# Kernel optimization log

Hardware: AMD Instinct MI355X
Metric: run time of the kernel (lower is better)

Reference implementation:

```python
import jax, jax.numpy as jnp
import numpy as np

B, N, D = 256, 2048, 256

def setup_inputs() -> dict:
    key = jax.random.key(0)
    k1, k2, k3, k4 = jax.random.split(key, 4)
    feature = jax.random.normal(k1, (B, N, D), dtype=jnp.float32)
    pointer_hidden_state = jax.random.normal(k2, (B, D), dtype=jnp.float32)
    # learned params (match torch.randn init)
    v = jax.random.normal(k3, (1, 1, D), dtype=jnp.float32)
    W = jax.random.normal(k4, (1, D, 2 * D), dtype=jnp.float32)
    return {"feature": feature, "pointer_hidden_state": pointer_hidden_state, "v": v, "W": W}

def reference(feature, pointer_hidden_state, v, W):
    # hidden: concat(feature, broadcast hidden state) -> [B, N, 2D]
    b, n, d = feature.shape
    h = jnp.broadcast_to(pointer_hidden_state[:, None, :], (b, n, d))
    hidden = jnp.concatenate([feature, h], axis=2)            # [B, N, 2D]
    # W @ hidden^T fused as einsum: [D, 2D] x [B, N, 2D] -> [B, N, D]
    pre = jnp.tanh(jnp.einsum('de,bne->bnd', W[0], hidden))
    # v . pre -> [B, N]
    scores = jnp.einsum('d,bnd->bn', v[0, 0], pre)
    attns = jax.nn.softmax(scores, axis=1)[:, None, :]        # [B, 1, N]
    return attns
```

## Files before the change

### kernel.cpp

```cpp
#include <hip/hip_runtime.h>
#include <hip/hip_fp16.h>

typedef _Float16 f16;
typedef _Float16 f16x4 __attribute__((ext_vector_type(4)));
typedef _Float16 f16x8 __attribute__((ext_vector_type(8)));
typedef float f32x4 __attribute__((ext_vector_type(4)));

#define NCH 64
#define CHB 32768
#define PLB 16384
#define PSTRIDE 524288

#define BAR()     asm volatile("s_waitcnt lgkmcnt(0)\n\ts_barrier" ::: "memory")
#define WAITV_(N) asm volatile("s_waitcnt vmcnt(" #N ")" ::: "memory")
#define WAITV(N)  WAITV_(N)

__global__ void prep_w(const float* __restrict__ W, f16* __restrict__ wbuf) {
    int idx = blockIdx.x * 256 + threadIdx.x;
    int d = idx >> 8, k = idx & 255;
    float w = W[d * 512 + k];
    int ct   = d >> 4;
    int lane = (d & 15) | (((k >> 3) & 3) << 4);
    int ks   = k >> 5;
    int j    = k & 7;
    wbuf[(((ks * 16 + ct) * 64) + lane) * 8 + j] = (f16)w;
}

__global__ void prep_c(const float* __restrict__ W, const float* __restrict__ h,
                       float* __restrict__ c) {
    __shared__ float hs[256];
    int b = blockIdx.x, d = threadIdx.x;
    hs[d] = h[b * 256 + d];
    __syncthreads();
    const float4* w4 = (const float4*)(W + d * 512 + 256);
    const float4* h4 = (const float4*)hs;
    float acc = 0.f;
#pragma unroll 8
    for (int e = 0; e < 64; ++e) {
        float4 a = w4[e], bb = h4[e];
        acc += a.x * bb.x + a.y * bb.y + a.z * bb.z + a.w * bb.w;
    }
    c[b * 256 + d] = acc;
}

__global__ __launch_bounds__(512, 2)
void main_gemm(const float* __restrict__ feat, const f16* __restrict__ wbuf,
               const float* __restrict__ cb, const float* __restrict__ vvec,
               float* __restrict__ psc) {
    __shared__ __align__(16) char rawb[2 * CHB];
    __shared__ __align__(16) char plnb[2 * PLB];

    const int tid = threadIdx.x;
    const int w = tid >> 6;
    const int l = tid & 63;
    const int g = l >> 4;
    const int lr = l & 15;
    const int rh = w >> 2;
    const int cg = w & 3;
    const int b = blockIdx.x;

    f16x8 wf[4][8];
    {
        const f16x8* wp = (const f16x8*)wbuf;
#pragma unroll
        for (int ct = 0; ct < 4; ++ct) {
            int ctg = cg * 4 + ct;
#pragma unroll
            for (int ks = 0; ks < 8; ++ks)
                wf[ct][ks] = wp[(ks * 16 + ctg) * 64 + l];
        }
    }
    float c_[4], v_[4];
#pragma unroll
    for (int ct = 0; ct < 4; ++ct) {
        c_[ct] = cb[b * 256 + (cg * 4 + ct) * 16 + lr];
        v_[ct] = vvec[(cg * 4 + ct) * 16 + lr];
    }

    const char* tbb = (const char*)(feat + (size_t)b * 2048 * 256);

#define ISSUE(u)                                                                   \
    {                                                                              \
        const char* nb = tbb + (size_t)(u) * CHB;                                  \
        char* Q = rawb + ((u) & 1) * CHB;                                          \
        _Pragma("unroll")                                                          \
        for (int i = 0; i < 4; ++i)                                                \
            __builtin_amdgcn_global_load_lds(                                      \
                (const __attribute__((address_space(1))) void*)(nb + i * 8192 + tid * 16), \
                (__attribute__((address_space(3))) void*)(Q + i * 8192 + tid * 16),\
                16, 0, 0);                                                         \
    }

    const int ck0 = (tid & 63) * 4;
    int cvt_off[4];
#pragma unroll
    for (int r = 0; r < 4; ++r) {
        int row = r * 8 + w;
        cvt_off[r] = (((row * 512 + (ck0 & ~7) * 2) ^ ((row & 7) << 4)) +
                      ((ck0 & 4) << 1));
    }

#define CVT(u)                                                                     \
    {                                                                              \
        const char* rp = rawb + ((u) & 1) * CHB;                                   \
        char* hq = plnb + ((u) & 1) * PLB;                                         \
        _Pragma("unroll")                                                          \
        for (int r = 0; r < 4; ++r) {                                              \
            f32x4 x = *(const f32x4*)(rp + r * 8192 + tid * 16);                   \
            f16x4 hv = {(f16)x[0], (f16)x[1], (f16)x[2], (f16)x[3]};               \
            *(f16x4*)(hq + cvt_off[r]) = hv;                                       \
        }                                                                          \
    }

    const int arow = rh * 16 + lr;
    const int aswz = (arow & 7) << 4;

    ISSUE(0); ISSUE(1);
    WAITV(4);
    CVT(0);

    for (int t = 0; t < NCH; ++t) {
        BAR();
        if (t + 2 < NCH) ISSUE(t + 2);

        const char* hp = plnb + (t & 1) * PLB;
        f32x4 acc[4] = {};
#pragma unroll
        for (int ks = 0; ks < 8; ++ks) {
            int ao = (arow * 512 + ks * 64 + g * 16) ^ aswz;
            f16x8 ahi = *(const f16x8*)(hp + ao);
            acc[0] = __builtin_amdgcn_mfma_f32_16x16x32_f16(ahi, wf[0][ks], acc[0], 0, 0, 0);
            acc[1] = __builtin_amdgcn_mfma_f32_16x16x32_f16(ahi, wf[1][ks], acc[1], 0, 0, 0);
            acc[2] = __builtin_amdgcn_mfma_f32_16x16x32_f16(ahi, wf[2][ks], acc[2], 0, 0, 0);
            acc[3] = __builtin_amdgcn_mfma_f32_16x16x32_f16(ahi, wf[3][ks], acc[3], 0, 0, 0);
        }

        float s[4];
#pragma unroll
        for (int r = 0; r < 4; ++r) {
            float a = 0.f;
#pragma unroll
            for (int ct = 0; ct < 4; ++ct) {
                float x = acc[ct][r] + c_[ct];
                float tnh = 1.f - __fdividef(2.f, __expf(2.f * x) + 1.f);
                a += v_[ct] * tnh;
            }
            s[r] = a;
        }
#pragma unroll
        for (int m = 1; m < 16; m <<= 1) {
            s[0] += __shfl_xor(s[0], m, 64);
            s[1] += __shfl_xor(s[1], m, 64);
            s[2] += __shfl_xor(s[2], m, 64);
            s[3] += __shfl_xor(s[3], m, 64);
        }

        if (t < NCH - 2)      WAITV(4);
        else if (t == NCH - 2) WAITV(0);
        if (t + 1 < NCH) CVT(t + 1);

        if (lr == 0) {
            size_t rowg = (size_t)b * 2048 + t * 32 + rh * 16 + g * 4;
            float4 o = {s[0], s[1], s[2], s[3]};
            *(float4*)(psc + (size_t)cg * PSTRIDE + rowg) = o;
        }
    }
#undef ISSUE
#undef CVT
}

__global__ void softmax_k(const float* __restrict__ psc, float* __restrict__ out) {
    __shared__ float red[16];
    int b = blockIdx.x, tid = threadIdx.x;
    float sc[8];
    float m = -3.4e38f;
#pragma unroll
    for (int q = 0; q < 8; ++q) {
        size_t row = (size_t)b * 2048 + q * 256 + tid;
        sc[q] = (psc[row] + psc[PSTRIDE + row]) +
                (psc[2 * PSTRIDE + row] + psc[3 * PSTRIDE + row]);
        m = fmaxf(m, sc[q]);
    }
#pragma unroll
    for (int d = 1; d < 64; d <<= 1) m = fmaxf(m, __shfl_xor(m, d, 64));
    if ((tid & 63) == 0) red[tid >> 6] = m;
    __syncthreads();
    m = fmaxf(fmaxf(red[0], red[1]), fmaxf(red[2], red[3]));
    float e[8], sum = 0.f;
#pragma unroll
    for (int q = 0; q < 8; ++q) { e[q] = __expf(sc[q] - m); sum += e[q]; }
#pragma unroll
    for (int d = 1; d < 64; d <<= 1) sum += __shfl_xor(sum, d, 64);
    if ((tid & 63) == 0) red[8 + (tid >> 6)] = sum;
    __syncthreads();
    sum = (red[8] + red[9]) + (red[10] + red[11]);
    float inv = __fdividef(1.f, sum);
#pragma unroll
    for (int q = 0; q < 8; ++q)
        out[(size_t)b * 2048 + q * 256 + tid] = e[q] * inv;
}

extern "C" void kernel_launch(void* const* d_in, const int* in_sizes, int n_in,
                              void* d_out, int out_size, void* d_ws, size_t ws_size,
                              hipStream_t stream) {
    const float* feat = (const float*)d_in[0];
    const float* h    = (const float*)d_in[1];
    const float* v    = (const float*)d_in[2];
    const float* W    = (const float*)d_in[3];
    float* out = (float*)d_out;

    f16*   wbuf = (f16*)d_ws;
    float* cbuf = (float*)((char*)d_ws + 131072);
    float* psc  = (float*)((char*)d_ws + 524288);

    prep_w<<<256, 256, 0, stream>>>(W, wbuf);
    prep_c<<<256, 256, 0, stream>>>(W, h, cbuf);
    main_gemm<<<256, 512, 0, stream>>>(feat, wbuf, cbuf, v, psc);
    softmax_k<<<256, 256, 0, stream>>>(psc, out);
}
```

Before: 167.7 us.

## Fuse weight prep, bias compute, GEMM and softmax into a single kernel

Collapses four launches into one kernel. Each block now converts its W fragments to fp16 and computes its bias vector c from W and the hidden state, instead of relying on separate prep kernels. Partial scores are reduced across column groups in shared memory, and the softmax over N runs at the end of the same block, removing the global partial-score round trip and the separate softmax launch. In exchange, every block redundantly reads and converts W (256 blocks × 512 KB of mostly L2-resident data), and LDS usage rises by about 10 KB per block, which could affect the two-blocks-per-CU occupancy.

```diff
diff --git a/kernel.cpp b/kernel.cpp
--- a/kernel.cpp
+++ b/kernel.cpp
@@ -9,46 +9,22 @@
 #define NCH 64
 #define CHB 32768
 #define PLB 16384
-#define PSTRIDE 524288
 
 #define BAR()     asm volatile("s_waitcnt lgkmcnt(0)\n\ts_barrier" ::: "memory")
 #define WAITV_(N) asm volatile("s_waitcnt vmcnt(" #N ")" ::: "memory")
 #define WAITV(N)  WAITV_(N)
 
-__global__ void prep_w(const float* __restrict__ W, f16* __restrict__ wbuf) {
-    int idx = blockIdx.x * 256 + threadIdx.x;
-    int d = idx >> 8, k = idx & 255;
-    float w = W[d * 512 + k];
-    int ct   = d >> 4;
-    int lane = (d & 15) | (((k >> 3) & 3) << 4);
-    int ks   = k >> 5;
-    int j    = k & 7;
-    wbuf[(((ks * 16 + ct) * 64) + lane) * 8 + j] = (f16)w;
-}
-
-__global__ void prep_c(const float* __restrict__ W, const float* __restrict__ h,
-                       float* __restrict__ c) {
-    __shared__ float hs[256];
-    int b = blockIdx.x, d = threadIdx.x;
-    hs[d] = h[b * 256 + d];
-    __syncthreads();
-    const float4* w4 = (const float4*)(W + d * 512 + 256);
-    const float4* h4 = (const float4*)hs;
-    float acc = 0.f;
-#pragma unroll 8
-    for (int e = 0; e < 64; ++e) {
-        float4 a = w4[e], bb = h4[e];
-        acc += a.x * bb.x + a.y * bb.y + a.z * bb.z + a.w * bb.w;
-    }
-    c[b * 256 + d] = acc;
-}
-
 __global__ __launch_bounds__(512, 2)
-void main_gemm(const float* __restrict__ feat, const f16* __restrict__ wbuf,
-               const float* __restrict__ cb, const float* __restrict__ vvec,
-               float* __restrict__ psc) {
+void fused(const float* __restrict__ feat, const float* __restrict__ hvec,
+           const float* __restrict__ vvec, const float* __restrict__ W,
+           float* __restrict__ out) {
     __shared__ __align__(16) char rawb[2 * CHB];
     __shared__ __align__(16) char plnb[2 * PLB];
+    __shared__ __align__(16) float pbuf[2][32][4];
+    __shared__ __align__(16) float sbuf[2048];
+    __shared__ __align__(16) float hs[256];
+    __shared__ __align__(16) float cl[256];
+    __shared__ float red[16];
 
     const int tid = threadIdx.x;
     const int w = tid >> 6;
@@ -59,35 +35,56 @@
     const int cg = w & 3;
     const int b = blockIdx.x;
 
+    if (tid < 256) hs[tid] = hvec[b * 256 + tid];
+    __syncthreads();
+
+    {
+        int d = tid >> 1, half = tid & 1;
+        const float4* w4 = (const float4*)(W + d * 512 + 256 + half * 128);
+        const float4* h4 = (const float4*)(hs + half * 128);
+        float a = 0.f;
+#pragma unroll 8
+        for (int e = 0; e < 32; ++e) {
+            float4 x = w4[e], y = h4[e];
+            a += x.x * y.x + x.y * y.y + x.z * y.z + x.w * y.w;
+        }
+        a += __shfl_xor(a, 1, 64);
+        if (half == 0) cl[d] = a;
+    }
+
     f16x8 wf[4][8];
-    {
-        const f16x8* wp = (const f16x8*)wbuf;
-#pragma unroll
-        for (int ct = 0; ct < 4; ++ct) {
-            int ctg = cg * 4 + ct;
-#pragma unroll
-            for (int ks = 0; ks < 8; ++ks)
-                wf[ct][ks] = wp[(ks * 16 + ctg) * 64 + l];
-        }
-    }
-    float c_[4], v_[4];
 #pragma unroll
     for (int ct = 0; ct < 4; ++ct) {
-        c_[ct] = cb[b * 256 + (cg * 4 + ct) * 16 + lr];
-        v_[ct] = vvec[(cg * 4 + ct) * 16 + lr];
-    }
+        int d = (cg * 4 + ct) * 16 + lr;
+        const float* wr = W + d * 512 + g * 8;
+#pragma unroll
+        for (int ks = 0; ks < 8; ++ks) {
+            float4 a0 = *(const float4*)(wr + ks * 32);
+            float4 a1 = *(const float4*)(wr + ks * 32 + 4);
+            f16x8 hv = {(f16)a0.x, (f16)a0.y, (f16)a0.z, (f16)a0.w,
+                        (f16)a1.x, (f16)a1.y, (f16)a1.z, (f16)a1.w};
+            wf[ct][ks] = hv;
+        }
+    }
+    float v_[4];
+#pragma unroll
+    for (int ct = 0; ct < 4; ++ct) v_[ct] = vvec[(cg * 4 + ct) * 16 + lr];
+    __syncthreads();
+    float c_[4];
+#pragma unroll
+    for (int ct = 0; ct < 4; ++ct) c_[ct] = cl[(cg * 4 + ct) * 16 + lr];
 
     const char* tbb = (const char*)(feat + (size_t)b * 2048 * 256);
 
 #define ISSUE(u)                                                                   \
     {                                                                              \
-        const char* nb = tbb + (size_t)(u) * CHB;                                  \
-        char* Q = rawb + ((u) & 1) * CHB;                                          \
+        const char* nb_ = tbb + (size_t)(u) * CHB;                                 \
+        char* Q_ = rawb + ((u) & 1) * CHB;                                         \
         _Pragma("unroll")                                                          \
-        for (int i = 0; i < 4; ++i)                                                \
+        for (int i_ = 0; i_ < 4; ++i_)                                             \
             __builtin_amdgcn_global_load_lds(                                      \
-                (const __attribute__((address_space(1))) void*)(nb + i * 8192 + tid * 16), \
-                (__attribute__((address_space(3))) void*)(Q + i * 8192 + tid * 16),\
+                (const __attribute__((address_space(1))) void*)(nb_ + i_ * 8192 + tid * 16), \
+                (__attribute__((address_space(3))) void*)(Q_ + i_ * 8192 + tid * 16),\
                 16, 0, 0);                                                         \
     }
 
@@ -102,13 +99,13 @@
 
 #define CVT(u)                                                                     \
     {                                                                              \
-        const char* rp = rawb + ((u) & 1) * CHB;                                   \
-        char* hq = plnb + ((u) & 1) * PLB;                                         \
+        const char* rp_ = rawb + ((u) & 1) * CHB;                                  \
+        char* hq_ = plnb + ((u) & 1) * PLB;                                        \
         _Pragma("unroll")                                                          \
         for (int r = 0; r < 4; ++r) {                                              \
-            f32x4 x = *(const f32x4*)(rp + r * 8192 + tid * 16);                   \
-            f16x4 hv = {(f16)x[0], (f16)x[1], (f16)x[2], (f16)x[3]};               \
-            *(f16x4*)(hq + cvt_off[r]) = hv;                                       \
+            f32x4 x_ = *(const f32x4*)(rp_ + r * 8192 + tid * 16);                 \
+            f16x4 hv_ = {(f16)x_[0], (f16)x_[1], (f16)x_[2], (f16)x_[3]};          \
+            *(f16x4*)(hq_ + cvt_off[r]) = hv_;                                     \
         }                                                                          \
     }
 
@@ -122,6 +119,12 @@
     for (int t = 0; t < NCH; ++t) {
         BAR();
         if (t + 2 < NCH) ISSUE(t + 2);
+
+        if (t > 0 && w == ((t - 1) & 7) && l < 32) {
+            const float* pb_ = &pbuf[(t - 1) & 1][l][0];
+            f32x4 p_ = *(const f32x4*)pb_;
+            sbuf[(t - 1) * 32 + l] = (p_[0] + p_[1]) + (p_[2] + p_[3]);
+        }
 
         const char* hp = plnb + (t & 1) * PLB;
         f32x4 acc[4] = {};
@@ -160,44 +163,46 @@
         if (t + 1 < NCH) CVT(t + 1);
 
         if (lr == 0) {
-            size_t rowg = (size_t)b * 2048 + t * 32 + rh * 16 + g * 4;
-            float4 o = {s[0], s[1], s[2], s[3]};
-            *(float4*)(psc + (size_t)cg * PSTRIDE + rowg) = o;
+            int r0 = rh * 16 + g * 4;
+            pbuf[t & 1][r0 + 0][cg] = s[0];
+            pbuf[t & 1][r0 + 1][cg] = s[1];
+            pbuf[t & 1][r0 + 2][cg] = s[2];
+            pbuf[t & 1][r0 + 3][cg] = s[3];
         }
     }
 #undef ISSUE
 #undef CVT
-}
-
-__global__ void softmax_k(const float* __restrict__ psc, float* __restrict__ out) {
-    __shared__ float red[16];
-    int b = blockIdx.x, tid = threadIdx.x;
-    float sc[8];
-    float m = -3.4e38f;
-#pragma unroll
-    for (int q = 0; q < 8; ++q) {
-        size_t row = (size_t)b * 2048 + q * 256 + tid;
-        sc[q] = (psc[row] + psc[PSTRIDE + row]) +
-                (psc[2 * PSTRIDE + row] + psc[3 * PSTRIDE + row]);
-        m = fmaxf(m, sc[q]);
-    }
-#pragma unroll
-    for (int d = 1; d < 64; d <<= 1) m = fmaxf(m, __shfl_xor(m, d, 64));
-    if ((tid & 63) == 0) red[tid >> 6] = m;
-    __syncthreads();
-    m = fmaxf(fmaxf(red[0], red[1]), fmaxf(red[2], red[3]));
-    float e[8], sum = 0.f;
-#pragma unroll
-    for (int q = 0; q < 8; ++q) { e[q] = __expf(sc[q] - m); sum += e[q]; }
-#pragma unroll
-    for (int d = 1; d < 64; d <<= 1) sum += __shfl_xor(sum, d, 64);
-    if ((tid & 63) == 0) red[8 + (tid >> 6)] = sum;
-    __syncthreads();
-    sum = (red[8] + red[9]) + (red[10] + red[11]);
-    float inv = __fdividef(1.f, sum);
-#pragma unroll
-    for (int q = 0; q < 8; ++q)
-        out[(size_t)b * 2048 + q * 256 + tid] = e[q] * inv;
+
+    BAR();
+    if (w == ((NCH - 1) & 7) && l < 32) {
+        const float* pb_ = &pbuf[(NCH - 1) & 1][l][0];
+        f32x4 p_ = *(const f32x4*)pb_;
+        sbuf[(NCH - 1) * 32 + l] = (p_[0] + p_[1]) + (p_[2] + p_[3]);
+    }
+    BAR();
+
+    {
+        f32x4 x = *(const f32x4*)(sbuf + tid * 4);
+        float m = fmaxf(fmaxf(x[0], x[1]), fmaxf(x[2], x[3]));
+#pragma unroll
+        for (int d = 1; d < 64; d <<= 1) m = fmaxf(m, __shfl_xor(m, d, 64));
+        if (l == 0) red[w] = m;
+        __syncthreads();
+        m = fmaxf(fmaxf(fmaxf(red[0], red[1]), fmaxf(red[2], red[3])),
+                  fmaxf(fmaxf(red[4], red[5]), fmaxf(red[6], red[7])));
+        float e0 = __expf(x[0] - m), e1 = __expf(x[1] - m);
+        float e2 = __expf(x[2] - m), e3 = __expf(x[3] - m);
+        float sum = (e0 + e1) + (e2 + e3);
+#pragma unroll
+        for (int d = 1; d < 64; d <<= 1) sum += __shfl_xor(sum, d, 64);
+        if (l == 0) red[8 + w] = sum;
+        __syncthreads();
+        sum = ((red[8] + red[9]) + (red[10] + red[11])) +
+              ((red[12] + red[13]) + (red[14] + red[15]));
+        float inv = __fdividef(1.f, sum);
+        float4 o = {e0 * inv, e1 * inv, e2 * inv, e3 * inv};
+        *(float4*)(out + (size_t)b * 2048 + tid * 4) = o;
+    }
 }
 
 extern "C" void kernel_launch(void* const* d_in, const int* in_sizes, int n_in,
@@ -209,12 +214,5 @@
     const float* W    = (const float*)d_in[3];
     float* out = (float*)d_out;
 
-    f16*   wbuf = (f16*)d_ws;
-    float* cbuf = (float*)((char*)d_ws + 131072);
-    float* psc  = (float*)((char*)d_ws + 524288);
-
-    prep_w<<<256, 256, 0, stream>>>(W, wbuf);
-    prep_c<<<256, 256, 0, stream>>>(W, h, cbuf);
-    main_gemm<<<256, 512, 0, stream>>>(feat, wbuf, cbuf, v, psc);
-    softmax_k<<<256, 256, 0, stream>>>(psc, out);
+    fused<<<256, 512, 0, stream>>>(feat, h, v, W, out);
 }
```

Result: slower. 172.8 us (+3.0%).
